# Kernel optimization log

Measured on AMD Instinct MI355X. Metric: run time of the kernel, lower is better.

The kernel has to match this reference:

```python
import jax, jax.numpy as jnp
import numpy as np

N, E, G = 50000, 1600000, 8
IN, H, C = 64, 4, 32
HID = H * C  # 128
L = 3


def setup_inputs() -> dict:
    key = jax.random.key(0)
    ks = jax.random.split(key, 20)
    x = jax.random.normal(ks[0], (N, IN), dtype=jnp.float32)
    edge_index = jax.random.randint(ks[1], (2, E), 0, N, dtype=jnp.int64)
    batch = jnp.sort(jax.random.randint(ks[2], (N,), 0, G, dtype=jnp.int64))
    s = 0.05
    Wp = jax.random.normal(ks[3], (IN, HID), dtype=jnp.float32) * s
    bp = jnp.zeros((HID,), dtype=jnp.float32)
    Wl = jax.random.normal(ks[4], (L, HID, HID), dtype=jnp.float32) * s
    att_src = jax.random.normal(ks[5], (L, H, C), dtype=jnp.float32) * s
    att_dst = jax.random.normal(ks[6], (L, H, C), dtype=jnp.float32) * s
    bconv = jnp.zeros((L, HID), dtype=jnp.float32)
    W1 = jax.random.normal(ks[7], (2 * HID, 256), dtype=jnp.float32) * s
    b1 = jnp.zeros((256,), dtype=jnp.float32)
    W2 = jax.random.normal(ks[8], (256, 128), dtype=jnp.float32) * s
    b2 = jnp.zeros((128,), dtype=jnp.float32)
    W3 = jax.random.normal(ks[9], (128, 1), dtype=jnp.float32) * s
    b3 = jnp.zeros((1,), dtype=jnp.float32)
    return dict(x=x, edge_index=edge_index, batch=batch, Wp=Wp, bp=bp, Wl=Wl,
                att_src=att_src, att_dst=att_dst, bconv=bconv,
                W1=W1, b1=b1, W2=W2, b2=b2, W3=W3, b3=b3)


def _gat_layer(x, src, dst, W, a_src, a_dst, b):
    # PyG GATConv (concat=True, add_self_loops handled by caller via src/dst)
    h = (x @ W).reshape(N, H, C)                      # [N,H,C]
    asrc = jnp.sum(h * a_src, axis=-1)                # [N,H]
    adst = jnp.sum(h * a_dst, axis=-1)                # [N,H]
    e = jax.nn.leaky_relu(asrc[src] + adst[dst], 0.2)  # [E',H]
    m = jax.ops.segment_max(e, dst, num_segments=N)   # scatter-softmax over dst
    e = jnp.exp(e - m[dst])
    z = jax.ops.segment_sum(e, dst, num_segments=N)
    alpha = e / (z[dst] + 1e-16)                      # [E',H]
    out = jax.ops.segment_sum(h[src] * alpha[:, :, None], dst, num_segments=N)
    return out.reshape(N, HID) + b


def reference(x, edge_index, batch, Wp, bp, Wl, att_src, att_dst, bconv,
              W1, b1, W2, b2, W3, b3):
    # add self loops once (PyG default add_self_loops=True)
    loop = jnp.arange(N, dtype=edge_index.dtype)
    src = jnp.concatenate([edge_index[0], loop])
    dst = jnp.concatenate([edge_index[1], loop])

    h = jax.nn.relu(x @ Wp + bp)
    for l in range(L):
        h = jax.nn.relu(_gat_layer(h, src, dst, Wl[l], att_src[l], att_dst[l], bconv[l]))

    cnt = jax.ops.segment_sum(jnp.ones((N,), h.dtype), batch, num_segments=G)
    mean = jax.ops.segment_sum(h, batch, num_segments=G) / jnp.maximum(cnt, 1.0)[:, None]
    mx = jax.ops.segment_max(h, batch, num_segments=G)
    mx = jnp.where(cnt[:, None] > 0, mx, 0.0)
    p = jnp.concatenate([mean, mx], axis=-1)          # [G, 2*HID]

    p = jax.nn.relu(p @ W1 + b1)
    p = jax.nn.relu(p @ W2 + b2)
    return (p @ W3 + b3).squeeze(-1)                  # [G]
```

## Files before the change

kernel.cpp:

```cpp
#include <hip/hip_runtime.h>
#include <math.h>

#define NN 50000
#define GG 8
#define HEADS 4
#define CH 32
#define HID 128
#define NLAYER 3
#define POOL_S 64
#define DEG_CAP 96
#define NBG2 ((NN + 63) / 64)
#define NBS 1024

typedef __attribute__((ext_vector_type(8))) short bf16x8;
typedef __attribute__((ext_vector_type(4))) float f32x4;

__device__ float g_h[(size_t)NN * HID];
__device__ __attribute__((aligned(16))) unsigned short g_h2b[(size_t)NN * HID];
__device__ __attribute__((aligned(16))) unsigned short g_xhi[(size_t)NN * HID];
__device__ __attribute__((aligned(16))) unsigned short g_xlo[(size_t)NN * HID];
__device__ __attribute__((aligned(16))) unsigned short g_wthi[(size_t)NLAYER * HID * HID];
__device__ __attribute__((aligned(16))) unsigned short g_wtlo[(size_t)NLAYER * HID * HID];
__device__ float g_as[(size_t)NN * HEADS];
__device__ float g_ad[(size_t)NN * HEADS];
__device__ int g_cursor[NN];
__device__ __attribute__((aligned(16))) unsigned short g_csr16[(size_t)NN * DEG_CAP];
__device__ int g_starts[GG + 1];
__device__ double g_psum[(size_t)GG * POOL_S * HID];
__device__ float g_pmax[(size_t)GG * POOL_S * HID];

__device__ __forceinline__ float lrelu(float v) { return v > 0.f ? v : 0.2f * v; }

__device__ __forceinline__ float bf2f(unsigned short u) {
    union { unsigned int i; float f; } v;
    v.i = ((unsigned int)u) << 16;
    return v.f;
}
__device__ __forceinline__ unsigned short f2bf(float f) {
    union { float f; unsigned int i; } v;
    v.f = f;
    unsigned int r = v.i + 0x7FFFu + ((v.i >> 16) & 1u);
    return (unsigned short)(r >> 16);
}

__global__ void zero_kernel() {
    int i = blockIdx.x * blockDim.x + threadIdx.x;
    if (i < NN) g_cursor[i] = 0;
}

__global__ void wprep_kernel(const float* __restrict__ Wl) {
    int idx = blockIdx.x * 256 + threadIdx.x;
    if (idx >= NLAYER * HID * HID) return;
    int lay = idx / (HID * HID);
    int rem = idx - lay * HID * HID;
    int n = rem >> 7, k = rem & 127;
    float v = Wl[(size_t)lay * HID * HID + (size_t)k * HID + n];
    unsigned short h = f2bf(v);
    float r = v - bf2f(h);
    g_wthi[idx] = h;
    g_wtlo[idx] = f2bf(r);
}

template <int K>
__device__ __forceinline__ void proj_body(
    const float* __restrict__ Xp, const float* __restrict__ W, const float* __restrict__ bias,
    int blk) {
    constexpr int KT = 32;
    constexpr int XS = 68;
    __shared__ float Ws[KT * 128];
    __shared__ float Xs[KT * XS];
    int tid = threadIdx.x;
    int base = blk * 64;
    int rows = NN - base;
    if (rows > 64) rows = 64;
    int cg = tid & 15, rg = tid >> 4;
    int c0 = cg * 8, r0 = rg * 4;
    float acc[4][8];
#pragma unroll
    for (int i = 0; i < 4; i++)
#pragma unroll
        for (int j = 0; j < 8; j++) acc[i][j] = 0.f;

    for (int kb = 0; kb < K; kb += KT) {
        {
            const float4* Wg = (const float4*)(W + (size_t)kb * 128);
            float4* Ws4 = (float4*)Ws;
#pragma unroll
            for (int u = 0; u < 4; u++) Ws4[tid + u * 256] = Wg[tid + u * 256];
        }
#pragma unroll
        for (int u = 0; u < 2; u++) {
            int i = tid + u * 256;
            int r = i >> 3, k4 = i & 7;
            float4 v = {0.f, 0.f, 0.f, 0.f};
            if (r < rows) v = *(const float4*)(Xp + (size_t)(base + r) * K + kb + k4 * 4);
            Xs[(k4 * 4 + 0) * XS + r] = v.x;
            Xs[(k4 * 4 + 1) * XS + r] = v.y;
            Xs[(k4 * 4 + 2) * XS + r] = v.z;
            Xs[(k4 * 4 + 3) * XS + r] = v.w;
        }
        __syncthreads();
#pragma unroll 8
        for (int k = 0; k < KT; k++) {
            const float4 xa = *(const float4*)&Xs[k * XS + r0];
            const float4 wa = *(const float4*)&Ws[k * 128 + c0];
            const float4 wb = *(const float4*)&Ws[k * 128 + c0 + 4];
            const float xr[4] = {xa.x, xa.y, xa.z, xa.w};
            const float wr[8] = {wa.x, wa.y, wa.z, wa.w, wb.x, wb.y, wb.z, wb.w};
#pragma unroll
            for (int ii = 0; ii < 4; ii++)
#pragma unroll
                for (int jj = 0; jj < 8; jj++) acc[ii][jj] += xr[ii] * wr[jj];
        }
        __syncthreads();
    }

    float bv[8];
#pragma unroll
    for (int j = 0; j < 8; j++) bv[j] = bias[c0 + j];
#pragma unroll
    for (int ii = 0; ii < 4; ii++) {
        int r = r0 + ii;
        if (r < rows) {
            ushort4 h0, l0, h1, l1;
            float o[8];
#pragma unroll
            for (int jj = 0; jj < 8; jj++) o[jj] = fmaxf(acc[ii][jj] + bv[jj], 0.f);
            h0.x = f2bf(o[0]); h0.y = f2bf(o[1]); h0.z = f2bf(o[2]); h0.w = f2bf(o[3]);
            h1.x = f2bf(o[4]); h1.y = f2bf(o[5]); h1.z = f2bf(o[6]); h1.w = f2bf(o[7]);
            l0.x = f2bf(o[0] - bf2f(h0.x)); l0.y = f2bf(o[1] - bf2f(h0.y));
            l0.z = f2bf(o[2] - bf2f(h0.z)); l0.w = f2bf(o[3] - bf2f(h0.w));
            l1.x = f2bf(o[4] - bf2f(h1.x)); l1.y = f2bf(o[5] - bf2f(h1.y));
            l1.z = f2bf(o[6] - bf2f(h1.z)); l1.w = f2bf(o[7] - bf2f(h1.w));
            size_t off = (size_t)(base + r) * 128 + c0;
            *(ushort4*)&g_xhi[off] = h0;
            *(ushort4*)&g_xhi[off + 4] = h1;
            *(ushort4*)&g_xlo[off] = l0;
            *(ushort4*)&g_xlo[off + 4] = l1;
        }
    }
}

__device__ __forceinline__ void mfma_att_body(
    const float* __restrict__ att_s, const float* __restrict__ att_d,
    int lay, int blk) {
    __shared__ float Ysh[64][HID];
    int tid = threadIdx.x;
    int w = tid >> 6, l = tid & 63;
    int base = blk * 64;
    int rows = NN - base;
    if (rows > 64) rows = 64;
    int ar = l & 15, kg = l >> 4;
    int arow = base + w * 16 + ar;
    if (arow >= NN) arow = NN - 1;
    const unsigned short* xh = g_xhi + (size_t)arow * HID + kg * 8;
    const unsigned short* xl = g_xlo + (size_t)arow * HID + kg * 8;
    const unsigned short* wh = g_wthi + (size_t)lay * HID * HID + (size_t)ar * HID + kg * 8;
    const unsigned short* wl = g_wtlo + (size_t)lay * HID * HID + (size_t)ar * HID + kg * 8;

    f32x4 acc[8];
#pragma unroll
    for (int ct = 0; ct < 8; ct++) acc[ct] = (f32x4){0.f, 0.f, 0.f, 0.f};

#pragma unroll
    for (int ks = 0; ks < 4; ks++) {
        bf16x8 ah = *(const bf16x8*)(xh + ks * 32);
        bf16x8 al = *(const bf16x8*)(xl + ks * 32);
#pragma unroll
        for (int ct = 0; ct < 8; ct++) {
            bf16x8 bh = *(const bf16x8*)(wh + ct * 16 * HID + ks * 32);
            bf16x8 bl = *(const bf16x8*)(wl + ct * 16 * HID + ks * 32);
            acc[ct] = __builtin_amdgcn_mfma_f32_16x16x32_bf16(ah, bh, acc[ct], 0, 0, 0);
            acc[ct] = __builtin_amdgcn_mfma_f32_16x16x32_bf16(al, bh, acc[ct], 0, 0, 0);
            acc[ct] = __builtin_amdgcn_mfma_f32_16x16x32_bf16(ah, bl, acc[ct], 0, 0, 0);
        }
    }

#pragma unroll
    for (int ct = 0; ct < 8; ct++)
#pragma unroll
        for (int j = 0; j < 4; j++)
            Ysh[w * 16 + kg * 4 + j][ct * 16 + ar] = acc[ct][j];
    __syncthreads();

    int cg = tid & 15, rg = tid >> 4;
    int c0 = cg * 8, r0 = rg * 4;
    float avs[8], avd[8];
#pragma unroll
    for (int j = 0; j < 8; j++) { avs[j] = att_s[c0 + j]; avd[j] = att_d[c0 + j]; }
#pragma unroll
    for (int ii = 0; ii < 4; ii++) {
        int r = r0 + ii;
        float o[8];
#pragma unroll
        for (int jj = 0; jj < 8; jj++) o[jj] = Ysh[r][c0 + jj];
        if (r < rows) {
            uint4 pk;
            pk.x = (unsigned)f2bf(o[0]) | ((unsigned)f2bf(o[1]) << 16);
            pk.y = (unsigned)f2bf(o[2]) | ((unsigned)f2bf(o[3]) << 16);
            pk.z = (unsigned)f2bf(o[4]) | ((unsigned)f2bf(o[5]) << 16);
            pk.w = (unsigned)f2bf(o[6]) | ((unsigned)f2bf(o[7]) << 16);
            *(uint4*)&g_h2b[(size_t)(base + r) * 128 + c0] = pk;
        }
        float ps = 0.f, pd = 0.f;
#pragma unroll
        for (int jj = 0; jj < 8; jj++) { ps += o[jj] * avs[jj]; pd += o[jj] * avd[jj]; }
        ps += __shfl_xor(ps, 1); ps += __shfl_xor(ps, 2);
        pd += __shfl_xor(pd, 1); pd += __shfl_xor(pd, 2);
        if ((cg & 3) == 0 && r < rows) {
            g_as[(size_t)(base + r) * 4 + (cg >> 2)] = ps;
            g_ad[(size_t)(base + r) * 4 + (cg >> 2)] = pd;
        }
    }
}

__device__ __forceinline__ void scatter_body(
    const int* __restrict__ srcv, const int* __restrict__ dstv,
    int ebeg, int eend, int blk, int nblk) {
    int idx = ebeg + blk * 256 + threadIdx.x;
    int stride = nblk * 256;
    for (int j = idx; j < eend; j += stride) {
        int d = dstv[j];
        int pos = atomicAdd(&g_cursor[d], 1);
        if (pos < DEG_CAP) g_csr16[(size_t)d * DEG_CAP + pos] = (unsigned short)srcv[j];
    }
}

__global__ __launch_bounds__(256) void fat1_kernel(
    const float* __restrict__ Xp, const float* __restrict__ W, const float* __restrict__ bias,
    const int* __restrict__ srcv, const int* __restrict__ dstv, int ebeg, int eend) {
    if (blockIdx.x < NBG2) proj_body<64>(Xp, W, bias, blockIdx.x);
    else scatter_body(srcv, dstv, ebeg, eend, blockIdx.x - NBG2, gridDim.x - NBG2);
}

__global__ __launch_bounds__(256, 2) void fat2_kernel(
    const float* __restrict__ att_s, const float* __restrict__ att_d,
    const int* __restrict__ srcv, const int* __restrict__ dstv, int ebeg, int eend) {
    if (blockIdx.x < NBG2) mfma_att_body(att_s, att_d, 0, blockIdx.x);
    else scatter_body(srcv, dstv, ebeg, eend, blockIdx.x - NBG2, gridDim.x - NBG2);
}

__global__ __launch_bounds__(256, 2) void att_gemm_kernel(
    const float* __restrict__ att_s, const float* __restrict__ att_d, int lay) {
    mfma_att_body(att_s, att_d, lay, blockIdx.x);
}

template <bool LAST>
__global__ __launch_bounds__(256) void gat_layer_kernel(const float* __restrict__ bconv) {
    int wave = threadIdx.x >> 6;
    int lane = threadIdx.x & 63;
    int i = blockIdx.x * 4 + wave;

    int deg = g_cursor[i];
    if (deg > DEG_CAP) deg = DEG_CAP;

    int stream = lane >> 5;
    int sl = lane & 31;
    int hl = sl >> 3;
    int li = sl & 7;
    int c0 = sl * 4;
    int bsel = lane & 56;

    float ad_h = g_ad[(size_t)i * 4 + hl];
    const unsigned short* csr = &g_csr16[(size_t)i * DEG_CAP];

    float4 acc = {0.f, 0.f, 0.f, 0.f};
    float zraw = 0.f;

    int nfull = deg >> 4;
    for (int t = 0; t < nfull; ++t) {
        int j0 = t * 16 + stream * 8;
        uint4 cs = *(const uint4*)(csr + j0);
        int s0 = cs.x & 0xFFFF, s1 = cs.x >> 16;
        int s2 = cs.y & 0xFFFF, s3 = cs.y >> 16;
        int s4 = cs.z & 0xFFFF, s5 = cs.z >> 16;
        int s6 = cs.w & 0xFFFF, s7 = cs.w >> 16;
        ushort4 q0 = *(const ushort4*)&g_h2b[(s0 << 7) + c0];
        ushort4 q1 = *(const ushort4*)&g_h2b[(s1 << 7) + c0];
        ushort4 q2 = *(const ushort4*)&g_h2b[(s2 << 7) + c0];
        ushort4 q3 = *(const ushort4*)&g_h2b[(s3 << 7) + c0];
        ushort4 q4 = *(const ushort4*)&g_h2b[(s4 << 7) + c0];
        ushort4 q5 = *(const ushort4*)&g_h2b[(s5 << 7) + c0];
        ushort4 q6 = *(const ushort4*)&g_h2b[(s6 << 7) + c0];
        ushort4 q7 = *(const ushort4*)&g_h2b[(s7 << 7) + c0];
        unsigned wsel = li < 4 ? (li < 2 ? cs.x : cs.y) : (li < 6 ? cs.z : cs.w);
        int sm = (li & 1) ? (int)(wsel >> 16) : (int)(wsel & 0xFFFF);
        float a = g_as[(sm << 2) + hl];
        float wr = expf(lrelu(a + ad_h));
        zraw += wr;
        float w0 = __shfl(wr, bsel | 0);
        float w1 = __shfl(wr, bsel | 1);
        float w2 = __shfl(wr, bsel | 2);
        float w3 = __shfl(wr, bsel | 3);
        float w4 = __shfl(wr, bsel | 4);
        float w5 = __shfl(wr, bsel | 5);
        float w6 = __shfl(wr, bsel | 6);
        float w7 = __shfl(wr, bsel | 7);
        acc.x += w0 * bf2f(q0.x); acc.y += w0 * bf2f(q0.y); acc.z += w0 * bf2f(q0.z); acc.w += w0 * bf2f(q0.w);
        acc.x += w1 * bf2f(q1.x); acc.y += w1 * bf2f(q1.y); acc.z += w1 * bf2f(q1.z); acc.w += w1 * bf2f(q1.w);
        acc.x += w2 * bf2f(q2.x); acc.y += w2 * bf2f(q2.y); acc.z += w2 * bf2f(q2.z); acc.w += w2 * bf2f(q2.w);
        acc.x += w3 * bf2f(q3.x); acc.y += w3 * bf2f(q3.y); acc.z += w3 * bf2f(q3.z); acc.w += w3 * bf2f(q3.w);
        acc.x += w4 * bf2f(q4.x); acc.y += w4 * bf2f(q4.y); acc.z += w4 * bf2f(q4.z); acc.w += w4 * bf2f(q4.w);
        acc.x += w5 * bf2f(q5.x); acc.y += w5 * bf2f(q5.y); acc.z += w5 * bf2f(q5.z); acc.w += w5 * bf2f(q5.w);
        acc.x += w6 * bf2f(q6.x); acc.y += w6 * bf2f(q6.y); acc.z += w6 * bf2f(q6.z); acc.w += w6 * bf2f(q6.w);
        acc.x += w7 * bf2f(q7.x); acc.y += w7 * bf2f(q7.y); acc.z += w7 * bf2f(q7.z); acc.w += w7 * bf2f(q7.w);
    }

    int tbase = nfull * 16 + stream * 8;
#pragma unroll
    for (int k = 0; k < 8; ++k) {
        if (tbase + k < deg) {
            int s = csr[tbase + k];
            float a = g_as[(s << 2) + hl];
            float wr = expf(lrelu(a + ad_h));
            zraw += wr * 0.125f;
            ushort4 q = *(const ushort4*)&g_h2b[(s << 7) + c0];
            acc.x += wr * bf2f(q.x); acc.y += wr * bf2f(q.y);
            acc.z += wr * bf2f(q.z); acc.w += wr * bf2f(q.w);
        }
    }

    acc.x += __shfl_xor(acc.x, 32);
    acc.y += __shfl_xor(acc.y, 32);
    acc.z += __shfl_xor(acc.z, 32);
    acc.w += __shfl_xor(acc.w, 32);
    zraw += __shfl_xor(zraw, 1);
    zraw += __shfl_xor(zraw, 2);
    zraw += __shfl_xor(zraw, 4);
    zraw += __shfl_xor(zraw, 32);

    if (lane < 32) {
        float as_i = g_as[(i << 2) + hl];
        float sw = expf(lrelu(as_i + ad_h));
        float invz = 1.f / (zraw + sw + 1e-16f);
        ushort4 qs = *(const ushort4*)&g_h2b[(i << 7) + c0];
        float4 bc = *(const float4*)&bconv[c0];
        float4 o;
        o.x = fmaxf((sw * bf2f(qs.x) + acc.x) * invz + bc.x, 0.f);
        o.y = fmaxf((sw * bf2f(qs.y) + acc.y) * invz + bc.y, 0.f);
        o.z = fmaxf((sw * bf2f(qs.z) + acc.z) * invz + bc.z, 0.f);
        o.w = fmaxf((sw * bf2f(qs.w) + acc.w) * invz + bc.w, 0.f);
        if (LAST) {
            *(float4*)&g_h[(size_t)i * 128 + c0] = o;
        } else {
            ushort4 hh, ll;
            hh.x = f2bf(o.x); hh.y = f2bf(o.y); hh.z = f2bf(o.z); hh.w = f2bf(o.w);
            ll.x = f2bf(o.x - bf2f(hh.x)); ll.y = f2bf(o.y - bf2f(hh.y));
            ll.z = f2bf(o.z - bf2f(hh.z)); ll.w = f2bf(o.w - bf2f(hh.w));
            *(ushort4*)&g_xhi[(size_t)i * 128 + c0] = hh;
            *(ushort4*)&g_xlo[(size_t)i * 128 + c0] = ll;
        }
    }
}

__global__ void bounds_kernel(const int* __restrict__ batch) {
    int t = threadIdx.x;
    if (t > GG) return;
    int lo = 0, hi = NN;
    while (lo < hi) {
        int mid = (lo + hi) >> 1;
        if (batch[mid] < t) lo = mid + 1; else hi = mid;
    }
    g_starts[t] = lo;
}

__global__ void pool1_kernel() {
    int g = blockIdx.x / POOL_S, s = blockIdx.x % POOL_S;
    int n0 = g_starts[g], n1 = g_starts[g + 1];
    long long cnt = n1 - n0;
    int a = n0 + (int)(cnt * s / POOL_S);
    int b = n0 + (int)(cnt * (s + 1) / POOL_S);
    int c = threadIdx.x;
    double sum = 0.0;
    float mx = -INFINITY;
    for (int nn = a; nn < b; nn++) {
        float v = g_h[(size_t)nn * 128 + c];
        sum += v;
        mx = fmaxf(mx, v);
    }
    g_psum[(size_t)blockIdx.x * 128 + c] = sum;
    g_pmax[(size_t)blockIdx.x * 128 + c] = mx;
}

__global__ __launch_bounds__(256) void head_kernel(
    const float* __restrict__ W1, const float* __restrict__ b1,
    const float* __restrict__ W2, const float* __restrict__ b2,
    const float* __restrict__ W3, const float* __restrict__ b3,
    float* __restrict__ outv) {
    __shared__ float p[256];
    __shared__ float r1[256];
    __shared__ float r2[128];
    int g = blockIdx.x, t = threadIdx.x;
    int cnt = g_starts[g + 1] - g_starts[g];
    if (t < 128) {
        double s = 0.0;
        for (int q = 0; q < POOL_S; q++) s += g_psum[(size_t)(g * POOL_S + q) * 128 + t];
        double dcnt = cnt > 0 ? (double)cnt : 1.0;
        p[t] = (float)(s / dcnt);
    } else {
        int c = t - 128;
        float mx = -INFINITY;
        for (int q = 0; q < POOL_S; q++) mx = fmaxf(mx, g_pmax[(size_t)(g * POOL_S + q) * 128 + c]);
        p[t] = cnt > 0 ? mx : 0.f;
    }
    __syncthreads();
    float acc = b1[t];
    for (int k = 0; k < 256; k++) acc += p[k] * W1[k * 256 + t];
    r1[t] = fmaxf(acc, 0.f);
    __syncthreads();
    if (t < 128) {
        float a2 = b2[t];
        for (int k = 0; k < 256; k++) a2 += r1[k] * W2[k * 128 + t];
        r2[t] = fmaxf(a2, 0.f);
    }
    __syncthreads();
    if (t < 64) {
        float a3 = r2[t] * W3[t] + r2[t + 64] * W3[t + 64];
#pragma unroll
        for (int d = 32; d >= 1; d >>= 1) a3 += __shfl_down(a3, d);
        if (t == 0) outv[g] = a3 + b3[0];
    }
}

extern "C" void kernel_launch(void* const* d_in, const int* in_sizes, int n_in,
                              void* d_out, int out_size, void* d_ws, size_t ws_size,
                              hipStream_t stream) {
    const float* x = (const float*)d_in[0];
    const int* eidx = (const int*)d_in[1];
    const int* batch = (const int*)d_in[2];
    const float* Wp = (const float*)d_in[3];
    const float* bp = (const float*)d_in[4];
    const float* Wl = (const float*)d_in[5];
    const float* att_src = (const float*)d_in[6];
    const float* att_dst = (const float*)d_in[7];
    const float* bconv = (const float*)d_in[8];
    const float* W1 = (const float*)d_in[9];
    const float* b1 = (const float*)d_in[10];
    const float* W2 = (const float*)d_in[11];
    const float* b2 = (const float*)d_in[12];
    const float* W3 = (const float*)d_in[13];
    const float* b3 = (const float*)d_in[14];
    float* out = (float*)d_out;
    int E = in_sizes[1] / 2;
    int Emid = E / 2;

    zero_kernel<<<(NN + 255) / 256, 256, 0, stream>>>();
    wprep_kernel<<<(NLAYER * HID * HID + 255) / 256, 256, 0, stream>>>(Wl);

    fat1_kernel<<<NBG2 + NBS, 256, 0, stream>>>(x, Wp, bp, eidx, eidx + E, 0, Emid);

    fat2_kernel<<<NBG2 + NBS, 256, 0, stream>>>(att_src, att_dst, eidx, eidx + E, Emid, E);

    gat_layer_kernel<false><<<NN / 4, 256, 0, stream>>>(bconv);

    att_gemm_kernel<<<NBG2, 256, 0, stream>>>(
        att_src + (size_t)1 * HEADS * CH, att_dst + (size_t)1 * HEADS * CH, 1);
    gat_layer_kernel<false><<<NN / 4, 256, 0, stream>>>(bconv + (size_t)1 * HID);

    att_gemm_kernel<<<NBG2, 256, 0, stream>>>(
        att_src + (size_t)2 * HEADS * CH, att_dst + (size_t)2 * HEADS * CH, 2);
    gat_layer_kernel<true><<<NN / 4, 256, 0, stream>>>(bconv + (size_t)2 * HID);

    bounds_kernel<<<1, 64, 0, stream>>>(batch);
    pool1_kernel<<<GG * POOL_S, 128, 0, stream>>>();
    head_kernel<<<GG, 256, 0, stream>>>(W1, b1, W2, b2, W3, b3, out);
}
```

Before: 541.4 us.

## Scatter all edges in first fused kernel and unroll scatter loop by four

```diff
diff --git a/kernel.cpp b/kernel.cpp
--- a/kernel.cpp
+++ b/kernel.cpp
@@ -141,12 +141,48 @@
     }
 }
 
-__device__ __forceinline__ void mfma_att_body(
-    const float* __restrict__ att_s, const float* __restrict__ att_d,
-    int lay, int blk) {
+__device__ __forceinline__ void scatter_body(
+    const int* __restrict__ srcv, const int* __restrict__ dstv, int E, int blk, int nblk) {
+    int stride = nblk * 256;
+    int j = blk * 256 + threadIdx.x;
+    for (; j + 3 * stride < E; j += 4 * stride) {
+        int d0 = dstv[j];
+        int d1 = dstv[j + stride];
+        int d2 = dstv[j + 2 * stride];
+        int d3 = dstv[j + 3 * stride];
+        int s0 = srcv[j];
+        int s1 = srcv[j + stride];
+        int s2 = srcv[j + 2 * stride];
+        int s3 = srcv[j + 3 * stride];
+        int p0 = atomicAdd(&g_cursor[d0], 1);
+        int p1 = atomicAdd(&g_cursor[d1], 1);
+        int p2 = atomicAdd(&g_cursor[d2], 1);
+        int p3 = atomicAdd(&g_cursor[d3], 1);
+        if (p0 < DEG_CAP) g_csr16[(size_t)d0 * DEG_CAP + p0] = (unsigned short)s0;
+        if (p1 < DEG_CAP) g_csr16[(size_t)d1 * DEG_CAP + p1] = (unsigned short)s1;
+        if (p2 < DEG_CAP) g_csr16[(size_t)d2 * DEG_CAP + p2] = (unsigned short)s2;
+        if (p3 < DEG_CAP) g_csr16[(size_t)d3 * DEG_CAP + p3] = (unsigned short)s3;
+    }
+    for (; j < E; j += stride) {
+        int d = dstv[j];
+        int pos = atomicAdd(&g_cursor[d], 1);
+        if (pos < DEG_CAP) g_csr16[(size_t)d * DEG_CAP + pos] = (unsigned short)srcv[j];
+    }
+}
+
+__global__ __launch_bounds__(256) void fat1_kernel(
+    const float* __restrict__ Xp, const float* __restrict__ W, const float* __restrict__ bias,
+    const int* __restrict__ srcv, const int* __restrict__ dstv, int E) {
+    if (blockIdx.x < NBG2) proj_body<64>(Xp, W, bias, blockIdx.x);
+    else scatter_body(srcv, dstv, E, blockIdx.x - NBG2, NBS);
+}
+
+__global__ __launch_bounds__(256, 2) void att_gemm_kernel(
+    const float* __restrict__ att_s, const float* __restrict__ att_d, int lay) {
     __shared__ float Ysh[64][HID];
     int tid = threadIdx.x;
     int w = tid >> 6, l = tid & 63;
+    int blk = blockIdx.x;
     int base = blk * 64;
     int rows = NN - base;
     if (rows > 64) rows = 64;
@@ -212,37 +248,6 @@
             g_ad[(size_t)(base + r) * 4 + (cg >> 2)] = pd;
         }
     }
-}
-
-__device__ __forceinline__ void scatter_body(
-    const int* __restrict__ srcv, const int* __restrict__ dstv,
-    int ebeg, int eend, int blk, int nblk) {
-    int idx = ebeg + blk * 256 + threadIdx.x;
-    int stride = nblk * 256;
-    for (int j = idx; j < eend; j += stride) {
-        int d = dstv[j];
-        int pos = atomicAdd(&g_cursor[d], 1);
-        if (pos < DEG_CAP) g_csr16[(size_t)d * DEG_CAP + pos] = (unsigned short)srcv[j];
-    }
-}
-
-__global__ __launch_bounds__(256) void fat1_kernel(
-    const float* __restrict__ Xp, const float* __restrict__ W, const float* __restrict__ bias,
-    const int* __restrict__ srcv, const int* __restrict__ dstv, int ebeg, int eend) {
-    if (blockIdx.x < NBG2) proj_body<64>(Xp, W, bias, blockIdx.x);
-    else scatter_body(srcv, dstv, ebeg, eend, blockIdx.x - NBG2, gridDim.x - NBG2);
-}
-
-__global__ __launch_bounds__(256, 2) void fat2_kernel(
-    const float* __restrict__ att_s, const float* __restrict__ att_d,
-    const int* __restrict__ srcv, const int* __restrict__ dstv, int ebeg, int eend) {
-    if (blockIdx.x < NBG2) mfma_att_body(att_s, att_d, 0, blockIdx.x);
-    else scatter_body(srcv, dstv, ebeg, eend, blockIdx.x - NBG2, gridDim.x - NBG2);
-}
-
-__global__ __launch_bounds__(256, 2) void att_gemm_kernel(
-    const float* __restrict__ att_s, const float* __restrict__ att_d, int lay) {
-    mfma_att_body(att_s, att_d, lay, blockIdx.x);
 }
 
 template <bool LAST>
@@ -442,23 +447,21 @@
     const float* b3 = (const float*)d_in[14];
     float* out = (float*)d_out;
     int E = in_sizes[1] / 2;
-    int Emid = E / 2;
 
     zero_kernel<<<(NN + 255) / 256, 256, 0, stream>>>();
     wprep_kernel<<<(NLAYER * HID * HID + 255) / 256, 256, 0, stream>>>(Wl);
 
-    fat1_kernel<<<NBG2 + NBS, 256, 0, stream>>>(x, Wp, bp, eidx, eidx + E, 0, Emid);
-
-    fat2_kernel<<<NBG2 + NBS, 256, 0, stream>>>(att_src, att_dst, eidx, eidx + E, Emid, E);
-
+    fat1_kernel<<<NBG2 + NBS, 256, 0, stream>>>(x, Wp, bp, eidx, eidx + E, E);
+
+    att_gemm_kernel<<<NBG2, 256, 0, stream>>>(att_src, att_dst, 0);
     gat_layer_kernel<false><<<NN / 4, 256, 0, stream>>>(bconv);
 
     att_gemm_kernel<<<NBG2, 256, 0, stream>>>(
-        att_src + (size_t)1 * HEADS * CH, att_dst + (size_t)1 * HEADS * CH, 1);
+        att_src + (size_t)1 * HID, att_dst + (size_t)1 * HID, 1);
     gat_layer_kernel<false><<<NN / 4, 256, 0, stream>>>(bconv + (size_t)1 * HID);
 
     att_gemm_kernel<<<NBG2, 256, 0, stream>>>(
-        att_src + (size_t)2 * HEADS * CH, att_dst + (size_t)2 * HEADS * CH, 2);
+        att_src + (size_t)2 * HID, att_dst + (size_t)2 * HID, 2);
     gat_layer_kernel<true><<<NN / 4, 256, 0, stream>>>(bconv + (size_t)2 * HID);
 
     bounds_kernel<<<1, 64, 0, stream>>>(batch);
```

After: 602.4 us. 11.3% more time.
